# Kernel tuning notes

Hardware: AMD Instinct MI355X
Metric: run time of the kernel (lower is better)

The kernel has to match this reference:

```python
import jax, jax.numpy as jnp
import numpy as np

B, N, D, E, H = 16, 256, 64, 64, 8


def setup_inputs() -> dict:
    key = jax.random.key(0)
    ks = jax.random.split(key, 16)
    s = 0.05
    return {
        "query": jax.random.normal(ks[0], (B, N, D), jnp.float32),
        "edges_augmented": jax.random.normal(ks[1], (B, N, N, E), jnp.float32),
        "Wq": jax.random.normal(ks[2], (D, H * D), jnp.float32) * s,
        "bq": jnp.zeros((H * D,), jnp.float32),
        "Wk": jax.random.normal(ks[3], (D, H * D), jnp.float32) * s,
        "bk": jnp.zeros((H * D,), jnp.float32),
        "Wv": jax.random.normal(ks[4], (D, H * D), jnp.float32) * s,
        "bv": jnp.zeros((H * D,), jnp.float32),
        "Wa": jax.random.normal(ks[5], (E, H), jnp.float32) * s,
        "ba": jnp.zeros((H,), jnp.float32),
        "Wg": jax.random.normal(ks[6], (E, H), jnp.float32) * s,
        "bg": jnp.zeros((H,), jnp.float32),
        "Wo": jax.random.normal(ks[7], (H * D, D), jnp.float32) * s,
        "bo": jnp.zeros((D,), jnp.float32),
        "We": jax.random.normal(ks[8], (H, E), jnp.float32) * s,
        "be": jnp.zeros((E,), jnp.float32),
    }


def reference(query, edges_augmented, Wq, bq, Wk, bk, Wv, bv, Wa, ba, Wg, bg, Wo, bo, We, be):
    b, n, d = query.shape
    h = Wa.shape[1]
    # QKV projections -> [b, h, n, d]
    Q = (query @ Wq + bq).reshape(b, n, h, d).transpose(0, 2, 1, 3)
    Kt = (query @ Wk + bk).reshape(b, n, h, d).transpose(0, 2, 1, 3)
    V = (query @ Wv + bv).reshape(b, n, h, d).transpose(0, 2, 1, 3)
    scores = jnp.einsum('bhnd,bhmd->bhnm', Q, Kt) / jnp.sqrt(jnp.asarray(d, query.dtype))
    # edge-derived additive bias: [b,n,n,h] -> [b,h,n,n]
    attn_bias = (edges_augmented @ Wa + ba).transpose(0, 3, 1, 2)
    scores = scores + attn_bias
    # sigmoid gate on values
    g = jax.nn.sigmoid((edges_augmented @ Wg + bg).transpose(0, 3, 1, 2))  # [b,h,n,n]
    Vg = jnp.einsum('bhnm,bhmd->bhnd', g, V)
    attn = jax.nn.softmax(scores, axis=-1)
    out = jnp.einsum('bhnm,bhmd->bhnd', attn, Vg)
    out = out.transpose(0, 2, 1, 3).reshape(b, n, h * d)
    attention_output = out @ Wo + bo  # [b, n, d]
    # edges output: scores [b,h,n,m] -> [b,m,n,h] -> Dense to E
    edges_output = scores.transpose(0, 3, 2, 1) @ We + be  # [b, n, n, E]
    return (attention_output, edges_output)
```

## Files before the change

### kernel.cpp

```cpp
#include <hip/hip_runtime.h>

#define BB 16
#define NN 256
#define DD 64
#define EE 64
#define HH 8

typedef __attribute__((ext_vector_type(4))) float f32x4;
typedef __attribute__((ext_vector_type(8))) short short8;

__device__ __forceinline__ void fma4(float* acc, float x, float4 w) {
    acc[0] += x * w.x; acc[1] += x * w.y; acc[2] += x * w.z; acc[3] += x * w.w;
}

__device__ __forceinline__ unsigned short f2bf(float f) {
    union { float f; unsigned u; } v; v.f = f;
    unsigned r = v.u + 0x7FFFu + ((v.u >> 16) & 1u);
    return (unsigned short)(r >> 16);
}

__global__ __launch_bounds__(256) void qkv_kernel(
    const float* __restrict__ query,
    const float* __restrict__ Wq, const float* __restrict__ bq,
    const float* __restrict__ Wk, const float* __restrict__ bk,
    const float* __restrict__ Wv, const float* __restrict__ bv,
    unsigned short* __restrict__ Qb, unsigned short* __restrict__ Kb,
    unsigned short* __restrict__ Vtb)
{
    __shared__ __align__(16) float q_l[8][64];
    const int mtx = blockIdx.x >> 9;
    const int rem = blockIdx.x & 511;
    const int b   = rem >> 5;
    const int n0  = (rem & 31) << 3;
    const int tid = threadIdx.x;

    if (tid < 128)
        ((float4*)&q_l[0][0])[tid] =
            ((const float4*)(query + (size_t)(b * NN + n0) * DD))[tid];

    const int w    = tid >> 6;
    const int lane = tid & 63;
    const int r0   = w * 2;
    const float* W  = (mtx == 0) ? Wq : (mtx == 1) ? Wk : Wv;
    const float* bs = (mtx == 0) ? bq : (mtx == 1) ? bk : bv;

    const int c0 = lane << 2;
    float acc[2][2][4];
    {
        const float4 b0 = *(const float4*)(bs + c0);
        const float4 b1 = *(const float4*)(bs + 256 + c0);
        acc[0][0][0]=b0.x; acc[0][0][1]=b0.y; acc[0][0][2]=b0.z; acc[0][0][3]=b0.w;
        acc[0][1][0]=b1.x; acc[0][1][1]=b1.y; acc[0][1][2]=b1.z; acc[0][1][3]=b1.w;
        acc[1][0][0]=b0.x; acc[1][0][1]=b0.y; acc[1][0][2]=b0.z; acc[1][0][3]=b0.w;
        acc[1][1][0]=b1.x; acc[1][1][1]=b1.y; acc[1][1][2]=b1.z; acc[1][1][3]=b1.w;
    }
    __syncthreads();

    #pragma unroll 2
    for (int d4 = 0; d4 < 16; ++d4) {
        const float4 qa = ((const float4*)&q_l[r0][0])[d4];
        const float4 qb = ((const float4*)&q_l[r0 + 1][0])[d4];
        const float qav[4] = {qa.x, qa.y, qa.z, qa.w};
        const float qbv[4] = {qb.x, qb.y, qb.z, qb.w};
        #pragma unroll
        for (int k = 0; k < 4; ++k) {
            const float4 w0 = *(const float4*)(W + (size_t)(d4 * 4 + k) * 512 + c0);
            const float4 w1 = *(const float4*)(W + (size_t)(d4 * 4 + k) * 512 + 256 + c0);
            fma4(acc[0][0], qav[k], w0); fma4(acc[0][1], qav[k], w1);
            fma4(acc[1][0], qbv[k], w0); fma4(acc[1][1], qbv[k], w1);
        }
    }

    const int hq = lane >> 4;
    const int d0 = (lane & 15) << 2;
    if (mtx < 2) {
        unsigned short* T = (mtx == 0) ? Qb : Kb;
        const float scale = (mtx == 0) ? 0.125f : 1.0f;
        #pragma unroll
        for (int r = 0; r < 2; ++r)
            #pragma unroll
            for (int j = 0; j < 2; ++j) {
                const int h = j * 4 + hq;
                const unsigned int lo = (unsigned)f2bf(acc[r][j][0] * scale)
                                      | ((unsigned)f2bf(acc[r][j][1] * scale) << 16);
                const unsigned int hi = (unsigned)f2bf(acc[r][j][2] * scale)
                                      | ((unsigned)f2bf(acc[r][j][3] * scale) << 16);
                uint2* p = (uint2*)(T + ((size_t)(b * HH + h) * NN + n0 + r0 + r) * DD + d0);
                *p = make_uint2(lo, hi);
            }
    } else {
        #pragma unroll
        for (int r = 0; r < 2; ++r)
            #pragma unroll
            for (int j = 0; j < 2; ++j) {
                const int h = j * 4 + hq;
                #pragma unroll
                for (int k = 0; k < 4; ++k)
                    Vtb[((size_t)(b * HH + h) * DD + d0 + k) * NN + n0 + r0 + r] =
                        f2bf(acc[r][j][k]);
            }
    }
}

__global__ __launch_bounds__(256) void qk_kernel(
    const unsigned short* __restrict__ Qb, const unsigned short* __restrict__ Kb,
    float* __restrict__ scores)
{
    const int bh = blockIdx.x >> 3;
    const int nt = (blockIdx.x >> 1) & 3;
    const int mh = blockIdx.x & 1;
    const int tid = threadIdx.x;
    const int w = tid >> 6, l = tid & 63;
    const int lr = l & 15, lg = l >> 4;
    const int n0 = nt * 64 + w * 16;

    const unsigned short* qp = Qb + ((size_t)bh * NN + n0 + lr) * DD + lg * 8;
    const unsigned short* kp = Kb + ((size_t)bh * NN + mh * 128 + lr) * DD + lg * 8;

    const short8 a0 = *(const short8*)qp;
    const short8 a1 = *(const short8*)(qp + 32);

    f32x4 acc[8];
    #pragma unroll
    for (int mt = 0; mt < 8; ++mt) acc[mt] = (f32x4){0.f, 0.f, 0.f, 0.f};

    #pragma unroll
    for (int mt = 0; mt < 8; ++mt) {
        const short8 b0 = *(const short8*)(kp + (size_t)mt * 16 * DD);
        const short8 b1 = *(const short8*)(kp + (size_t)mt * 16 * DD + 32);
        acc[mt] = __builtin_amdgcn_mfma_f32_16x16x32_bf16(a0, b0, acc[mt], 0, 0, 0);
        acc[mt] = __builtin_amdgcn_mfma_f32_16x16x32_bf16(a1, b1, acc[mt], 0, 0, 0);
    }

    float* sp = scores + (size_t)bh * NN * NN;
    #pragma unroll
    for (int mt = 0; mt < 8; ++mt)
        #pragma unroll
        for (int r = 0; r < 4; ++r)
            sp[(size_t)(n0 + lg * 4 + r) * NN + mh * 128 + mt * 16 + lr] = acc[mt][r];
}

__global__ __launch_bounds__(256) void edges_kernel(
    const float* __restrict__ edges,
    const float* __restrict__ Wa, const float* __restrict__ ba,
    const float* __restrict__ Wg, const float* __restrict__ bg,
    const float* __restrict__ We, const float* __restrict__ be,
    float* __restrict__ scores,
    unsigned short* __restrict__ gates,
    float* __restrict__ edges_out)
{
    __shared__ __align__(16) unsigned short eb[128 * 64];
    __shared__ __align__(16) unsigned short wc[16 * 64];
    __shared__ __align__(16) float bgl[128][20];
    __shared__ float bal[8], bgb[8];

    const int mh  = blockIdx.x & 1;
    const int n   = (blockIdx.x >> 1) & 255;
    const int b   = blockIdx.x >> 9;
    const int m0  = mh << 7;
    const int tid = threadIdx.x;
    const int w   = tid >> 6, l = tid & 63;
    const int lr  = l & 15, lg = l >> 4;

    const int fm = tid & 127;
    const int fh = (tid >> 7) << 2;
    const size_t so0 = ((size_t)(b * HH + fh) << 16) + ((size_t)n << 8) + m0 + fm;
    float qk[4];
    #pragma unroll
    for (int i = 0; i < 4; ++i) qk[i] = scores[so0 + ((size_t)i << 16)];

    float wecol[8];
    #pragma unroll
    for (int h = 0; h < 8; ++h) wecol[h] = We[h * EE + l];
    const float bev = be[l];

    #pragma unroll
    for (int j = 0; j < 4; ++j) {
        const int idx = tid * 4 + j;
        const int hp = idx >> 6, e = idx & 63;
        const float v = (hp < 8) ? Wa[e * 8 + hp] : Wg[e * 8 + (hp - 8)];
        *(unsigned short*)((char*)wc + hp * 128 + ((e * 2) ^ ((hp & 7) << 4))) = f2bf(v);
    }
    if (tid < 8) { bal[tid] = ba[tid]; bgb[tid] = bg[tid]; }

    const f32x4* esrc = (const f32x4*)(edges + ((size_t)(b * NN + n) * NN + m0) * DD);
    #pragma unroll
    for (int it = 0; it < 8; ++it) {
        const int c = it * 256 + tid;
        const f32x4 x = __builtin_nontemporal_load(esrc + c);
        const int m = c >> 4, e4 = c & 15;
        const unsigned lo = (unsigned)f2bf(x[0]) | ((unsigned)f2bf(x[1]) << 16);
        const unsigned hi = (unsigned)f2bf(x[2]) | ((unsigned)f2bf(x[3]) << 16);
        *(uint2*)((char*)eb + m * 128 + ((e4 * 8) ^ ((m & 7) << 4))) = make_uint2(lo, hi);
    }
    __syncthreads();

    short8 bfrag[2];
    #pragma unroll
    for (int ks = 0; ks < 2; ++ks)
        bfrag[ks] = *(const short8*)((char*)wc + lr * 128 +
                                     ((ks * 64 + lg * 16) ^ ((lr & 7) << 4)));

    #pragma unroll
    for (int t = 0; t < 2; ++t) {
        const int T = w * 2 + t;
        f32x4 acc = (f32x4){0.f, 0.f, 0.f, 0.f};
        #pragma unroll
        for (int ks = 0; ks < 2; ++ks) {
            const int m = T * 16 + lr;
            const short8 af = *(const short8*)((char*)eb + m * 128 +
                                 ((ks * 64 + lg * 16) ^ ((lr & 7) << 4)));
            acc = __builtin_amdgcn_mfma_f32_16x16x32_bf16(af, bfrag[ks], acc, 0, 0, 0);
        }
        #pragma unroll
        for (int r = 0; r < 4; ++r)
            bgl[T * 16 + lg * 4 + r][lr] = acc[r];
    }
    __syncthreads();

    #pragma unroll
    for (int i = 0; i < 4; ++i) {
        const int h = fh + i;
        const float sc = qk[i] + bgl[fm][h] + bal[h];
        scores[so0 + ((size_t)i << 16)] = sc;
        bgl[fm][h] = sc;
        const float gv = bgl[fm][8 + h] + bgb[h];
        gates[so0 + ((size_t)i << 16)] = f2bf(1.f / (1.f + __expf(-gv)));
    }
    __syncthreads();

    #pragma unroll 4
    for (int mi = 0; mi < 32; ++mi) {
        const int m = w * 32 + mi;
        const float4 sa = *(const float4*)&bgl[m][0];
        const float4 sb = *(const float4*)&bgl[m][4];
        const float v = bev
            + sa.x * wecol[0] + sa.y * wecol[1] + sa.z * wecol[2] + sa.w * wecol[3]
            + sb.x * wecol[4] + sb.y * wecol[5] + sb.z * wecol[6] + sb.w * wecol[7];
        __builtin_nontemporal_store(v,
            edges_out + ((size_t)(b * NN + m0 + m) * NN + n) * DD + l);
    }
}

__global__ __launch_bounds__(256) void vg_kernel(
    const unsigned short* __restrict__ gates, const unsigned short* __restrict__ Vtb,
    unsigned short* __restrict__ Vgt)
{
    const int dh = blockIdx.x & 1;
    const int q  = (blockIdx.x >> 1) & 3;
    const int bh = blockIdx.x >> 3;
    const int tid = threadIdx.x;
    const int w = tid >> 6, l = tid & 63;
    const int lr = l & 15, lg = l >> 4;
    const int n0 = q * 64 + w * 16;

    const unsigned short* gp = gates + ((size_t)bh * NN + n0 + lr) * NN + lg * 8;
    const unsigned short* vp = Vtb + ((size_t)bh * DD + lr) * NN + lg * 8;

    f32x4 acc[2];
    #pragma unroll
    for (int dt = 0; dt < 2; ++dt) acc[dt] = (f32x4){0.f, 0.f, 0.f, 0.f};

    #pragma unroll
    for (int ks = 0; ks < 8; ++ks) {
        const short8 bfr = *(const short8*)(gp + ks * 32);
        #pragma unroll
        for (int dt = 0; dt < 2; ++dt) {
            const short8 afr = *(const short8*)(vp + (size_t)(dh * 2 + dt) * 16 * NN + ks * 32);
            acc[dt] = __builtin_amdgcn_mfma_f32_16x16x32_bf16(afr, bfr, acc[dt], 0, 0, 0);
        }
    }

    unsigned short* op = Vgt + (size_t)bh * DD * NN;
    #pragma unroll
    for (int dt = 0; dt < 2; ++dt)
        #pragma unroll
        for (int r = 0; r < 4; ++r)
            op[(size_t)((dh * 2 + dt) * 16 + lg * 4 + r) * NN + n0 + lr] = f2bf(acc[dt][r]);
}

__global__ __launch_bounds__(512) void out_kernel(
    const float* __restrict__ scores, const unsigned short* __restrict__ Vgt,
    const float* __restrict__ Wo, const float* __restrict__ bo,
    float* __restrict__ att_out)
{
    __shared__ float o_l[16][521];
    const int b  = blockIdx.x >> 4;
    const int nt = blockIdx.x & 15;
    const int n0 = nt * 16;
    const int tid = threadIdx.x;
    const int w = tid >> 6, l = tid & 63;
    const int lr = l & 15, lg = l >> 4;
    const int h = w;

    {
        const f32x4* sp = (const f32x4*)(scores +
            ((size_t)(b * HH + h) * NN + n0 + lr) * NN + lg * 8);
        float s[64];
        #pragma unroll
        for (int ks = 0; ks < 8; ++ks) {
            const f32x4 x0 = __builtin_nontemporal_load(sp + ks * 8);
            const f32x4 x1 = __builtin_nontemporal_load(sp + ks * 8 + 1);
            s[ks * 8 + 0] = x0[0]; s[ks * 8 + 1] = x0[1];
            s[ks * 8 + 2] = x0[2]; s[ks * 8 + 3] = x0[3];
            s[ks * 8 + 4] = x1[0]; s[ks * 8 + 5] = x1[1];
            s[ks * 8 + 6] = x1[2]; s[ks * 8 + 7] = x1[3];
        }
        float mx = -1e30f;
        #pragma unroll
        for (int i = 0; i < 64; ++i) mx = fmaxf(mx, s[i]);
        mx = fmaxf(mx, __shfl_xor(mx, 16, 64));
        mx = fmaxf(mx, __shfl_xor(mx, 32, 64));
        float sm = 0.f;
        #pragma unroll
        for (int i = 0; i < 64; ++i) { s[i] = __expf(s[i] - mx); sm += s[i]; }
        sm += __shfl_xor(sm, 16, 64);
        sm += __shfl_xor(sm, 32, 64);
        const float inv = 1.f / sm;

        const unsigned short* vp = Vgt + ((size_t)(b * HH + h) * DD + lr) * NN + lg * 8;
        f32x4 acc[4];
        #pragma unroll
        for (int dt = 0; dt < 4; ++dt) acc[dt] = (f32x4){0.f, 0.f, 0.f, 0.f};

        #pragma unroll
        for (int ks = 0; ks < 8; ++ks) {
            union { short8 v; unsigned short u[8]; } bf;
            #pragma unroll
            for (int j = 0; j < 8; ++j) bf.u[j] = f2bf(s[ks * 8 + j] * inv);
            #pragma unroll
            for (int dt = 0; dt < 4; ++dt) {
                const short8 afr = *(const short8*)(vp + (size_t)dt * 16 * NN + ks * 32);
                acc[dt] = __builtin_amdgcn_mfma_f32_16x16x32_bf16(afr, bf.v, acc[dt], 0, 0, 0);
            }
        }
        #pragma unroll
        for (int dt = 0; dt < 4; ++dt)
            #pragma unroll
            for (int r = 0; r < 4; ++r)
                o_l[lr][h * 64 + dt * 16 + lg * 4 + r] = acc[dt][r];
    }
    __syncthreads();

    const int n  = tid >> 5;
    const int d2 = (tid & 31) << 1;
    float a0 = bo[d2], a1 = bo[d2 + 1];
    const float* orow = &o_l[n][0];
    #pragma unroll 8
    for (int k = 0; k < 512; ++k) {
        const float o = orow[k];
        const float2 w2 = *(const float2*)(Wo + (size_t)k * 64 + d2);
        a0 += o * w2.x; a1 += o * w2.y;
    }
    *(float2*)(att_out + ((size_t)(b * NN + n0 + n)) * DD + d2) = make_float2(a0, a1);
}

extern "C" void kernel_launch(void* const* d_in, const int* in_sizes, int n_in,
                              void* d_out, int out_size, void* d_ws, size_t ws_size,
                              hipStream_t stream)
{
    const float* query = (const float*)d_in[0];
    const float* edges = (const float*)d_in[1];
    const float* Wq = (const float*)d_in[2];  const float* bq = (const float*)d_in[3];
    const float* Wk = (const float*)d_in[4];  const float* bk = (const float*)d_in[5];
    const float* Wv = (const float*)d_in[6];  const float* bv = (const float*)d_in[7];
    const float* Wa = (const float*)d_in[8];  const float* ba = (const float*)d_in[9];
    const float* Wg = (const float*)d_in[10]; const float* bg = (const float*)d_in[11];
    const float* Wo = (const float*)d_in[12]; const float* bo = (const float*)d_in[13];
    const float* We = (const float*)d_in[14]; const float* be = (const float*)d_in[15];

    float* att_out   = (float*)d_out;
    float* edges_out = (float*)d_out + 262144;

    char* base = (char*)d_ws;
    float*          scores = (float*)base;
    unsigned short* gates  = (unsigned short*)(base + 33554432);
    unsigned short* Qb     = (unsigned short*)(base + 50331648);
    unsigned short* Kb     = (unsigned short*)(base + 54525952);
    unsigned short* Vtb    = (unsigned short*)(base + 58720256);
    unsigned short* Vgt    = (unsigned short*)(base + 62914560);

    hipLaunchKernelGGL(qkv_kernel, dim3(1536), dim3(256), 0, stream,
                       query, Wq, bq, Wk, bk, Wv, bv, Qb, Kb, Vtb);
    hipLaunchKernelGGL(qk_kernel, dim3(1024), dim3(256), 0, stream,
                       Qb, Kb, scores);
    hipLaunchKernelGGL(edges_kernel, dim3(8192), dim3(256), 0, stream,
                       edges, Wa, ba, Wg, bg, We, be, scores, gates, edges_out);
    hipLaunchKernelGGL(vg_kernel, dim3(1024), dim3(256), 0, stream,
                       gates, Vtb, Vgt);
    hipLaunchKernelGGL(out_kernel, dim3(256), dim3(512), 0, stream,
                       scores, Vgt, Wo, bo, att_out);
}
```

Before: 575.8 us.

## Fuse QK score computation into edges kernel and prefetch edge tiles into registers

Removes the separate qk_kernel. Each edges block now computes its own row of Q·K scores with MFMA, using the single query row n broadcast across 16 lanes, and keeps them in shared memory instead of writing scores and reading them back from global. Edge loads are issued into registers before the QK MFMAs so the memory latency overlaps with that compute. The cost is that 15/16 of each MFMA output is wasted, K is reloaded for every n block, register pressure grows from holding 8 f32x4 values, and the bgl padding drops the 16-byte alignment so float4 reads become scalar reads.

```diff
diff --git a/kernel.cpp b/kernel.cpp
--- a/kernel.cpp
+++ b/kernel.cpp
@@ -102,46 +102,9 @@
     }
 }
 
-__global__ __launch_bounds__(256) void qk_kernel(
-    const unsigned short* __restrict__ Qb, const unsigned short* __restrict__ Kb,
-    float* __restrict__ scores)
-{
-    const int bh = blockIdx.x >> 3;
-    const int nt = (blockIdx.x >> 1) & 3;
-    const int mh = blockIdx.x & 1;
-    const int tid = threadIdx.x;
-    const int w = tid >> 6, l = tid & 63;
-    const int lr = l & 15, lg = l >> 4;
-    const int n0 = nt * 64 + w * 16;
-
-    const unsigned short* qp = Qb + ((size_t)bh * NN + n0 + lr) * DD + lg * 8;
-    const unsigned short* kp = Kb + ((size_t)bh * NN + mh * 128 + lr) * DD + lg * 8;
-
-    const short8 a0 = *(const short8*)qp;
-    const short8 a1 = *(const short8*)(qp + 32);
-
-    f32x4 acc[8];
-    #pragma unroll
-    for (int mt = 0; mt < 8; ++mt) acc[mt] = (f32x4){0.f, 0.f, 0.f, 0.f};
-
-    #pragma unroll
-    for (int mt = 0; mt < 8; ++mt) {
-        const short8 b0 = *(const short8*)(kp + (size_t)mt * 16 * DD);
-        const short8 b1 = *(const short8*)(kp + (size_t)mt * 16 * DD + 32);
-        acc[mt] = __builtin_amdgcn_mfma_f32_16x16x32_bf16(a0, b0, acc[mt], 0, 0, 0);
-        acc[mt] = __builtin_amdgcn_mfma_f32_16x16x32_bf16(a1, b1, acc[mt], 0, 0, 0);
-    }
-
-    float* sp = scores + (size_t)bh * NN * NN;
-    #pragma unroll
-    for (int mt = 0; mt < 8; ++mt)
-        #pragma unroll
-        for (int r = 0; r < 4; ++r)
-            sp[(size_t)(n0 + lg * 4 + r) * NN + mh * 128 + mt * 16 + lr] = acc[mt][r];
-}
-
 __global__ __launch_bounds__(256) void edges_kernel(
     const float* __restrict__ edges,
+    const unsigned short* __restrict__ Qb, const unsigned short* __restrict__ Kb,
     const float* __restrict__ Wa, const float* __restrict__ ba,
     const float* __restrict__ Wg, const float* __restrict__ bg,
     const float* __restrict__ We, const float* __restrict__ be,
@@ -151,7 +114,8 @@
 {
     __shared__ __align__(16) unsigned short eb[128 * 64];
     __shared__ __align__(16) unsigned short wc[16 * 64];
-    __shared__ __align__(16) float bgl[128][20];
+    __shared__ float bgl[128][17];
+    __shared__ float qk_l[8][132];
     __shared__ float bal[8], bgb[8];
 
     const int mh  = blockIdx.x & 1;
@@ -162,17 +126,34 @@
     const int w   = tid >> 6, l = tid & 63;
     const int lr  = l & 15, lg = l >> 4;
 
-    const int fm = tid & 127;
-    const int fh = (tid >> 7) << 2;
-    const size_t so0 = ((size_t)(b * HH + fh) << 16) + ((size_t)n << 8) + m0 + fm;
-    float qk[4];
-    #pragma unroll
-    for (int i = 0; i < 4; ++i) qk[i] = scores[so0 + ((size_t)i << 16)];
-
     float wecol[8];
     #pragma unroll
     for (int h = 0; h < 8; ++h) wecol[h] = We[h * EE + l];
     const float bev = be[l];
+
+    const f32x4* esrc = (const f32x4*)(edges + ((size_t)(b * NN + n) * NN + m0) * DD);
+    f32x4 xr[8];
+    #pragma unroll
+    for (int it = 0; it < 8; ++it)
+        xr[it] = __builtin_nontemporal_load(esrc + it * 256 + tid);
+
+    #pragma unroll
+    for (int hh = 0; hh < 2; ++hh) {
+        const int h = w * 2 + hh;
+        const unsigned short* qp = Qb + ((size_t)(b * HH + h) * NN + n) * DD + lg * 8;
+        const short8 qf0 = *(const short8*)qp;
+        const short8 qf1 = *(const short8*)(qp + 32);
+        const unsigned short* kp = Kb + ((size_t)(b * HH + h) * NN + m0 + lr) * DD + lg * 8;
+        #pragma unroll
+        for (int T = 0; T < 8; ++T) {
+            const short8 k0 = *(const short8*)(kp + (size_t)T * 16 * DD);
+            const short8 k1 = *(const short8*)(kp + (size_t)T * 16 * DD + 32);
+            f32x4 a = (f32x4){0.f, 0.f, 0.f, 0.f};
+            a = __builtin_amdgcn_mfma_f32_16x16x32_bf16(qf0, k0, a, 0, 0, 0);
+            a = __builtin_amdgcn_mfma_f32_16x16x32_bf16(qf1, k1, a, 0, 0, 0);
+            if (lg == 0) qk_l[h][T * 16 + lr] = a[0];
+        }
+    }
 
     #pragma unroll
     for (int j = 0; j < 4; ++j) {
@@ -183,14 +164,12 @@
     }
     if (tid < 8) { bal[tid] = ba[tid]; bgb[tid] = bg[tid]; }
 
-    const f32x4* esrc = (const f32x4*)(edges + ((size_t)(b * NN + n) * NN + m0) * DD);
     #pragma unroll
     for (int it = 0; it < 8; ++it) {
         const int c = it * 256 + tid;
-        const f32x4 x = __builtin_nontemporal_load(esrc + c);
         const int m = c >> 4, e4 = c & 15;
-        const unsigned lo = (unsigned)f2bf(x[0]) | ((unsigned)f2bf(x[1]) << 16);
-        const unsigned hi = (unsigned)f2bf(x[2]) | ((unsigned)f2bf(x[3]) << 16);
+        const unsigned lo = (unsigned)f2bf(xr[it][0]) | ((unsigned)f2bf(xr[it][1]) << 16);
+        const unsigned hi = (unsigned)f2bf(xr[it][2]) | ((unsigned)f2bf(xr[it][3]) << 16);
         *(uint2*)((char*)eb + m * 128 + ((e4 * 8) ^ ((m & 7) << 4))) = make_uint2(lo, hi);
     }
     __syncthreads();
@@ -218,25 +197,31 @@
     }
     __syncthreads();
 
-    #pragma unroll
-    for (int i = 0; i < 4; ++i) {
-        const int h = fh + i;
-        const float sc = qk[i] + bgl[fm][h] + bal[h];
-        scores[so0 + ((size_t)i << 16)] = sc;
-        bgl[fm][h] = sc;
-        const float gv = bgl[fm][8 + h] + bgb[h];
-        gates[so0 + ((size_t)i << 16)] = f2bf(1.f / (1.f + __expf(-gv)));
+    {
+        const int fm = tid & 127;
+        const int fh = (tid >> 7) << 2;
+        const size_t so0 = ((size_t)(b * HH + fh) << 16) + ((size_t)n << 8) + m0 + fm;
+        float qk4[4];
+        #pragma unroll
+        for (int i = 0; i < 4; ++i) qk4[i] = qk_l[fh + i][fm];
+        #pragma unroll
+        for (int i = 0; i < 4; ++i) {
+            const int h = fh + i;
+            const float sc = qk4[i] + bgl[fm][h] + bal[h];
+            scores[so0 + ((size_t)i << 16)] = sc;
+            bgl[fm][h] = sc;
+            const float gv = bgl[fm][8 + h] + bgb[h];
+            gates[so0 + ((size_t)i << 16)] = f2bf(1.f / (1.f + __expf(-gv)));
+        }
     }
     __syncthreads();
 
     #pragma unroll 4
     for (int mi = 0; mi < 32; ++mi) {
         const int m = w * 32 + mi;
-        const float4 sa = *(const float4*)&bgl[m][0];
-        const float4 sb = *(const float4*)&bgl[m][4];
-        const float v = bev
-            + sa.x * wecol[0] + sa.y * wecol[1] + sa.z * wecol[2] + sa.w * wecol[3]
-            + sb.x * wecol[4] + sb.y * wecol[5] + sb.z * wecol[6] + sb.w * wecol[7];
+        float v = bev;
+        #pragma unroll
+        for (int h = 0; h < 8; ++h) v += bgl[m][h] * wecol[h];
         __builtin_nontemporal_store(v,
             edges_out + ((size_t)(b * NN + m0 + m) * NN + n) * DD + l);
     }
@@ -382,10 +367,8 @@
 
     hipLaunchKernelGGL(qkv_kernel, dim3(1536), dim3(256), 0, stream,
                        query, Wq, bq, Wk, bk, Wv, bv, Qb, Kb, Vtb);
-    hipLaunchKernelGGL(qk_kernel, dim3(1024), dim3(256), 0, stream,
-                       Qb, Kb, scores);
     hipLaunchKernelGGL(edges_kernel, dim3(8192), dim3(256), 0, stream,
-                       edges, Wa, ba, Wg, bg, We, be, scores, gates, edges_out);
+                       edges, Qb, Kb, Wa, ba, Wg, bg, We, be, scores, gates, edges_out);
     hipLaunchKernelGGL(vg_kernel, dim3(1024), dim3(256), 0, stream,
                        gates, Vtb, Vgt);
     hipLaunchKernelGGL(out_kernel, dim3(256), dim3(512), 0, stream,
```

Measured after the change: 641.1 us. +11.3%, slower.
